# Optimization experiments

Measured on AMD Instinct MI355X. Metric: run time of the kernel, lower is better.

## Reference

```python
import jax, jax.numpy as jnp
import numpy as np

B = 64        # batch_size (conf.loader.batch_size)
N = 128       # points per graph
RATIO = 32    # aggregator nodes per graph
H = 8         # n_heads
HD = 64       # head dim = in_channels
E = H * HD    # embed dim = in_channels * n_heads = 512


def setup_inputs() -> dict:
    key = jax.random.key(0)
    ks = jax.random.split(key, 5)
    x = jax.random.normal(ks[0], (B, N, E), dtype=jnp.float32)
    # per-node graph ids, matching the row-major reshape of x: node i -> graph i // N
    batch = jnp.repeat(jnp.arange(B, dtype=jnp.int32), N)  # (B*N,)
    # learned aggregator seeds: torch.normal(0, 1, size=(ratio, E))
    aggrs = jax.random.normal(ks[1], (RATIO, E), dtype=jnp.float32)
    # MultiheadAttention params (torch layout: in_proj_weight (3E, E), out_proj (E, E))
    in_proj_w = jax.random.normal(ks[2], (3 * E, E), dtype=jnp.float32) / np.sqrt(E)
    in_proj_b = jnp.zeros((3 * E,), dtype=jnp.float32)
    out_proj_w = jax.random.normal(ks[3], (E, E), dtype=jnp.float32) / np.sqrt(E)
    out_proj_b = jnpp if False else jnp.zeros((E,), dtype=jnp.float32)
    return {"x": x, "batch": batch, "aggrs": aggrs,
            "in_proj_w": in_proj_w, "in_proj_b": in_proj_b,
            "out_proj_w": out_proj_w, "out_proj_b": out_proj_b}


def reference(x, batch, aggrs, in_proj_w, in_proj_b, out_proj_w, out_proj_b):
    Bsz, n, F = x.shape                       # (64, 128, 512)
    L = Bsz * RATIO                           # 2048 aggregator queries
    x_large = x.reshape(-1, F)                # (S, E), S = B*N = 8192
    q_in = jnp.tile(aggrs, (Bsz, 1))          # (L, E): aggrs.repeat(batch_size, 1)

    Wq, Wk, Wv = jnp.split(in_proj_w, 3, axis=0)
    bq, bk, bv = jnp.split(in_proj_b, 3)
    q = (q_in @ Wq.T + bq).reshape(L, H, HD).transpose(1, 0, 2)      # (H, L, HD)
    k = (x_large @ Wk.T + bk).reshape(-1, H, HD).transpose(1, 0, 2)  # (H, S, HD)
    v = (x_large @ Wv.T + bv).reshape(-1, H, HD).transpose(1, 0, 2)  # (H, S, HD)

    scores = jnp.einsum('hld,hsd->hls', q, k) / np.float32(np.sqrt(HD))  # (H, L, S)
    # mask = ~eye(B).repeat_interleave(ratio, 1); mask[batch].T -> (L, S) bool, True = blocked.
    # Equivalent: query l (belonging to graph l // ratio) may attend node s iff batch[s] == l // ratio.
    aggr_graph = jnp.arange(L, dtype=batch.dtype) // RATIO           # (L,)
    allowed = aggr_graph[:, None] == batch[None, :]                  # (L, S)
    scores = jnp.where(allowed[None, :, :], scores, -jnp.inf)
    attn = jax.nn.softmax(scores, axis=-1)                           # (H, L, S)

    out = jnp.einsum('hls,hsd->hld', attn, v)                        # (H, L, HD)
    out = out.transpose(1, 0, 2).reshape(L, F) @ out_proj_w.T + out_proj_b
    return out.reshape(Bsz, RATIO, F)                                # (B, ratio, E)
```

## Files before the change

kernel.cpp:

```cpp
#include <hip/hip_runtime.h>

typedef __attribute__((ext_vector_type(8))) short short8;
typedef __attribute__((ext_vector_type(4))) float f32x4;

__device__ inline float bf2f(unsigned short u) {
    return __uint_as_float(((unsigned int)u) << 16);
}
__device__ inline unsigned short f2bf(float f) {
    unsigned int x = __float_as_uint(f);
    return (unsigned short)((x + 0x7fffu + ((x >> 16) & 1u)) >> 16);
}

template<bool F32>
__device__ inline short8 load8(const void* p, long i) {
    short8 r;
    if (F32) {
        const float* fp = (const float*)p + i;
        f32x4 a = *(const f32x4*)fp;
        f32x4 b = *(const f32x4*)(fp + 4);
#pragma unroll
        for (int j = 0; j < 4; ++j) { r[j] = (short)f2bf(a[j]); r[4 + j] = (short)f2bf(b[j]); }
    } else {
        r = *(const short8*)((const unsigned short*)p + i);
    }
    return r;
}

__global__ __launch_bounds__(256) void prep_kernel(
    const float* __restrict__ w_in, const float* __restrict__ Wo,
    const float* __restrict__ aggrs, const float* __restrict__ b_in,
    const float* __restrict__ x,
    unsigned short* __restrict__ wkv,
    unsigned short* __restrict__ wob,
    unsigned short* __restrict__ Qs,
    unsigned short* __restrict__ xb)
{
    if (blockIdx.x < 8) {
        const int tid = threadIdx.x;
        const int w = tid >> 6, lane = tid & 63, l15 = lane & 15, l4 = lane >> 4;
        const int col0 = blockIdx.x * 64 + w * 16;
        const float bq = b_in[col0 + l15];
        for (int rt = 0; rt < 2; ++rt) {
            f32x4 acc = {0.f, 0.f, 0.f, 0.f};
#pragma unroll
            for (int kk = 0; kk < 16; ++kk) {
                short8 a = load8<true>(aggrs, (long)(rt * 16 + l15) * 512 + kk * 32 + l4 * 8);
                short8 b = load8<true>(w_in, (long)(col0 + l15) * 512 + kk * 32 + l4 * 8);
                acc = __builtin_amdgcn_mfma_f32_16x16x32_bf16(a, b, acc, 0, 0, 0);
            }
#pragma unroll
            for (int r = 0; r < 4; ++r)
                Qs[(long)(rt * 16 + l4 * 4 + r) * 512 + col0 + l15] = f2bf(acc[r] + bq);
        }
        return;
    }
    long u = (long)(blockIdx.x - 8) * 256 + threadIdx.x;
    const float* src;
    unsigned short* dst;
    long base;
    if (u < 65536)        { src = w_in + (long)512 * 512; dst = wkv; base = u; }
    else if (u < 98304)   { src = Wo;  dst = wob; base = u - 65536; }
    else if (u < 622592)  { src = x;   dst = xb;  base = u - 98304; }
    else return;
    long i = base * 8;
    f32x4 a = *(const f32x4*)(src + i);
    f32x4 b = *(const f32x4*)(src + i + 4);
    short8 v;
#pragma unroll
    for (int j = 0; j < 4; ++j) { v[j] = (short)f2bf(a[j]); v[4 + j] = (short)f2bf(b[j]); }
    *(short8*)(dst + i) = v;
}

__global__ __launch_bounds__(256, 2) void kvattn_kernel(
    const unsigned short* __restrict__ xb,
    const unsigned short* __restrict__ wkv,
    const float* __restrict__ b_in,
    const unsigned short* __restrict__ Qs,
    unsigned short* __restrict__ Oh)
{
    const int g = blockIdx.x;
    const int h = blockIdx.y;
    const int tid = threadIdx.x;
    const int w = tid >> 6, lane = tid & 63, l15 = lane & 15, l4 = lane >> 4;

    __shared__ __align__(16) unsigned short Wstage[16][512];
    __shared__ __align__(16) unsigned short K_lds[128][72];
    __shared__ __align__(16) unsigned short Vt_lds[64][136];
    __shared__ __align__(16) float S_lds[32][132];
    __shared__ __align__(16) unsigned short P_lds[32][136];

    short8 a0[16], a1[16];
    {
        const long xrow0 = (long)(g * 128 + w * 32 + l15) * 512 + l4 * 8;
#pragma unroll
        for (int kk = 0; kk < 16; ++kk) a0[kk] = *(const short8*)(xb + xrow0 + kk * 32);
        const long xrow1 = xrow0 + 16 * 512;
#pragma unroll
        for (int kk = 0; kk < 16; ++kk) a1[kk] = *(const short8*)(xb + xrow1 + kk * 32);
    }

    for (int cb = 0; cb < 8; ++cb) {
        if (cb) __syncthreads();
        const int wrow = (cb < 4) ? (h * 64 + cb * 16) : (512 + h * 64 + (cb - 4) * 16);
#pragma unroll
        for (int j = 0; j < 4; ++j) {
            int c = tid + j * 256;
            int row = c >> 6;
            int col8 = c & 63;
            *(short8*)(&Wstage[row][(col8 ^ (row & 7)) * 8]) =
                *(const short8*)(wkv + (long)(wrow + row) * 512 + col8 * 8);
        }
        __syncthreads();
        const float bias = b_in[512 + wrow + l15];
#pragma unroll
        for (int rt = 0; rt < 2; ++rt) {
            f32x4 acc = {0.f, 0.f, 0.f, 0.f};
#pragma unroll
            for (int kk = 0; kk < 16; ++kk) {
                short8 b = *(const short8*)(&Wstage[l15][((kk * 4 + l4) ^ (l15 & 7)) * 8]);
                acc = __builtin_amdgcn_mfma_f32_16x16x32_bf16(rt ? a1[kk] : a0[kk], b, acc, 0, 0, 0);
            }
            const int node0 = w * 32 + rt * 16 + l4 * 4;
            if (cb < 4) {
                const int col = cb * 16 + l15;
#pragma unroll
                for (int r = 0; r < 4; ++r) K_lds[node0 + r][col] = f2bf(acc[r] + bias);
            } else {
                const int d = (cb - 4) * 16 + l15;
#pragma unroll
                for (int r = 0; r < 4; ++r) Vt_lds[d][node0 + r] = f2bf(acc[r] + bias);
            }
        }
    }
    __syncthreads();

    for (int lt = 0; lt < 2; ++lt) {
        const int l0 = lt * 16;
        short8 qa[2];
        qa[0] = *(const short8*)(Qs + (long)(l0 + l15) * 512 + h * 64 + l4 * 8);
        qa[1] = *(const short8*)(Qs + (long)(l0 + l15) * 512 + h * 64 + 32 + l4 * 8);
        for (int ct = 0; ct < 2; ++ct) {
            const int n0 = w * 32 + ct * 16;
            f32x4 acc = {0.f, 0.f, 0.f, 0.f};
#pragma unroll
            for (int kk = 0; kk < 2; ++kk) {
                short8 b = *(const short8*)(&K_lds[n0 + l15][kk * 32 + l4 * 8]);
                acc = __builtin_amdgcn_mfma_f32_16x16x32_bf16(qa[kk], b, acc, 0, 0, 0);
            }
#pragma unroll
            for (int r = 0; r < 4; ++r)
                S_lds[l0 + l4 * 4 + r][n0 + l15] = acc[r] * 0.125f;
        }
    }
    __syncthreads();

    {
        const int row = tid >> 3;
        const int j = tid & 7;
        float vals[16];
        float m = -1e30f;
#pragma unroll
        for (int c = 0; c < 16; ++c) {
            vals[c] = S_lds[row][j + c * 8];
            m = fmaxf(m, vals[c]);
        }
#pragma unroll
        for (int s = 1; s < 8; s <<= 1) m = fmaxf(m, __shfl_xor(m, s));
        float sum = 0.f;
#pragma unroll
        for (int c = 0; c < 16; ++c) {
            vals[c] = __expf(vals[c] - m);
            sum += vals[c];
        }
#pragma unroll
        for (int s = 1; s < 8; s <<= 1) sum += __shfl_xor(sum, s);
        const float inv = 1.0f / sum;
#pragma unroll
        for (int c = 0; c < 16; ++c)
            P_lds[row][j + c * 8] = f2bf(vals[c] * inv);
    }
    __syncthreads();

    for (int lt = 0; lt < 2; ++lt) {
        const int l0 = lt * 16;
        const int d0 = w * 16;
        f32x4 acc = {0.f, 0.f, 0.f, 0.f};
#pragma unroll
        for (int kk = 0; kk < 4; ++kk) {
            short8 a = *(const short8*)(&P_lds[l0 + l15][kk * 32 + l4 * 8]);
            short8 b = *(const short8*)(&Vt_lds[d0 + l15][kk * 32 + l4 * 8]);
            acc = __builtin_amdgcn_mfma_f32_16x16x32_bf16(a, b, acc, 0, 0, 0);
        }
#pragma unroll
        for (int r = 0; r < 4; ++r) {
            const int l = l0 + l4 * 4 + r;
            Oh[(long)h * 131072 + (long)(g * 32 + l) * 64 + d0 + l15] = f2bf(acc[r]);
        }
    }
}

__global__ __launch_bounds__(256, 2) void outproj2_kernel(
    const unsigned short* __restrict__ Oh, const unsigned short* __restrict__ wob,
    const float* __restrict__ bo, float* __restrict__ out)
{
    const int by = blockIdx.x;
    const int tid = threadIdx.x;
    const int w = tid >> 6, lane = tid & 63, l15 = lane & 15, l4 = lane >> 4;

    __shared__ __align__(16) unsigned short O_lds[16][520];

#pragma unroll
    for (int i = 0; i < 4; ++i) {
        int c2 = tid + i * 256;
        int row = c2 >> 6;
        int c = c2 & 63;
        int hh = c >> 3;
        int d = (c & 7) * 8;
        *(short8*)(&O_lds[row][c * 8]) =
            *(const short8*)(Oh + (long)hh * 131072 + (long)(by * 16 + row) * 64 + d);
    }
    __syncthreads();

    short8 a[16];
#pragma unroll
    for (int kk = 0; kk < 16; ++kk)
        a[kk] = *(const short8*)(&O_lds[l15][kk * 32 + l4 * 8]);

    const int cbase = w * 128;
    for (int ct = 0; ct < 8; ++ct) {
        const int col0 = cbase + ct * 16;
        f32x4 acc = {0.f, 0.f, 0.f, 0.f};
#pragma unroll
        for (int kk = 0; kk < 16; ++kk) {
            short8 b = *(const short8*)(wob + (long)(col0 + l15) * 512 + kk * 32 + l4 * 8);
            acc = __builtin_amdgcn_mfma_f32_16x16x32_bf16(a[kk], b, acc, 0, 0, 0);
        }
        const float bias = bo[col0 + l15];
#pragma unroll
        for (int r = 0; r < 4; ++r)
            out[(long)(by * 16 + l4 * 4 + r) * 512 + col0 + l15] = acc[r] + bias;
    }
}

template<bool F32>
__device__ void attn_body(const void* x, const void* w_in, const float* b_in,
                          const void* aggrs, float* O) {
    const int h = blockIdx.x;
    const int g = blockIdx.y;
    const int tid = threadIdx.x;
    const int w = tid >> 6, lane = tid & 63, l15 = lane & 15, l4 = lane >> 4;

    __shared__ __align__(16) unsigned short Q_lds[32][72];
    __shared__ __align__(16) unsigned short K_lds[128][72];
    __shared__ __align__(16) unsigned short Vt_lds[64][136];
    __shared__ __align__(16) float S_lds[32][132];
    __shared__ __align__(16) unsigned short P_lds[32][136];

    const long xg = (long)g * 128 * 512;
    const long WqO = (long)(h * 64) * 512;
    const long WkO = (long)(512 + h * 64) * 512;
    const long WvO = (long)(1024 + h * 64) * 512;

    {
        const int d0 = w * 16;
        const float bq = b_in[h * 64 + d0 + l15];
        for (int rt = 0; rt < 2; ++rt) {
            f32x4 acc = {0.f, 0.f, 0.f, 0.f};
#pragma unroll
            for (int kk = 0; kk < 16; ++kk) {
                short8 a = load8<F32>(aggrs, (long)(rt * 16 + l15) * 512 + l4 * 8 + kk * 32);
                short8 b = load8<F32>(w_in, WqO + (long)(d0 + l15) * 512 + l4 * 8 + kk * 32);
                acc = __builtin_amdgcn_mfma_f32_16x16x32_bf16(a, b, acc, 0, 0, 0);
            }
#pragma unroll
            for (int r = 0; r < 4; ++r)
                Q_lds[rt * 16 + l4 * 4 + r][d0 + l15] = f2bf(acc[r] + bq);
        }
    }
    for (int rt = 0; rt < 2; ++rt) {
        const int n0 = w * 32 + rt * 16;
        short8 a[16];
#pragma unroll
        for (int kk = 0; kk < 16; ++kk)
            a[kk] = load8<F32>(x, xg + (long)(n0 + l15) * 512 + l4 * 8 + kk * 32);
        for (int ct = 0; ct < 4; ++ct) {
            const int d0 = ct * 16;
            f32x4 accK = {0.f, 0.f, 0.f, 0.f};
            f32x4 accV = {0.f, 0.f, 0.f, 0.f};
#pragma unroll
            for (int kk = 0; kk < 16; ++kk) {
                short8 bk = load8<F32>(w_in, WkO + (long)(d0 + l15) * 512 + l4 * 8 + kk * 32);
                short8 bv = load8<F32>(w_in, WvO + (long)(d0 + l15) * 512 + l4 * 8 + kk * 32);
                accK = __builtin_amdgcn_mfma_f32_16x16x32_bf16(a[kk], bk, accK, 0, 0, 0);
                accV = __builtin_amdgcn_mfma_f32_16x16x32_bf16(a[kk], bv, accV, 0, 0, 0);
            }
            const float biasK = b_in[512 + h * 64 + d0 + l15];
            const float biasV = b_in[1024 + h * 64 + d0 + l15];
#pragma unroll
            for (int r = 0; r < 4; ++r) {
                const int row = n0 + l4 * 4 + r;
                const int col = d0 + l15;
                K_lds[row][col] = f2bf(accK[r] + biasK);
                Vt_lds[col][row] = f2bf(accV[r] + biasV);
            }
        }
    }
    __syncthreads();
    for (int lt = 0; lt < 2; ++lt) {
        const int l0 = lt * 16;
        short8 qa[2];
        qa[0] = *(const short8*)(&Q_lds[l0 + l15][l4 * 8]);
        qa[1] = *(const short8*)(&Q_lds[l0 + l15][32 + l4 * 8]);
        for (int ct = 0; ct < 2; ++ct) {
            const int n0 = w * 32 + ct * 16;
            f32x4 acc = {0.f, 0.f, 0.f, 0.f};
#pragma unroll
            for (int kk = 0; kk < 2; ++kk) {
                short8 b = *(const short8*)(&K_lds[n0 + l15][kk * 32 + l4 * 8]);
                acc = __builtin_amdgcn_mfma_f32_16x16x32_bf16(qa[kk], b, acc, 0, 0, 0);
            }
#pragma unroll
            for (int r = 0; r < 4; ++r)
                S_lds[l0 + l4 * 4 + r][n0 + l15] = acc[r] * 0.125f;
        }
    }
    __syncthreads();
    {
        const int row = tid >> 3;
        const int j = tid & 7;
        float vals[16];
        float m = -1e30f;
#pragma unroll
        for (int c = 0; c < 16; ++c) {
            vals[c] = S_lds[row][j + c * 8];
            m = fmaxf(m, vals[c]);
        }
#pragma unroll
        for (int s = 1; s < 8; s <<= 1) m = fmaxf(m, __shfl_xor(m, s));
        float sum = 0.f;
#pragma unroll
        for (int c = 0; c < 16; ++c) {
            vals[c] = __expf(vals[c] - m);
            sum += vals[c];
        }
#pragma unroll
        for (int s = 1; s < 8; s <<= 1) sum += __shfl_xor(sum, s);
        const float inv = 1.0f / sum;
#pragma unroll
        for (int c = 0; c < 16; ++c)
            P_lds[row][j + c * 8] = f2bf(vals[c] * inv);
    }
    __syncthreads();
    for (int lt = 0; lt < 2; ++lt) {
        const int l0 = lt * 16;
        const int d0 = w * 16;
        f32x4 acc = {0.f, 0.f, 0.f, 0.f};
#pragma unroll
        for (int kk = 0; kk < 4; ++kk) {
            short8 a = *(const short8*)(&P_lds[l0 + l15][kk * 32 + l4 * 8]);
            short8 b = *(const short8*)(&Vt_lds[d0 + l15][kk * 32 + l4 * 8]);
            acc = __builtin_amdgcn_mfma_f32_16x16x32_bf16(a, b, acc, 0, 0, 0);
        }
#pragma unroll
        for (int r = 0; r < 4; ++r) {
            const int l = l0 + l4 * 4 + r;
            O[(long)(g * 32 + l) * 512 + h * 64 + d0 + l15] = acc[r];
        }
    }
}
__global__ __launch_bounds__(256) void attn_f32(const float* x, const float* w_in,
                                                const float* b_in, const float* aggrs,
                                                float* O) {
    attn_body<true>(x, w_in, b_in, aggrs, O);
}

template<bool F32>
__device__ void outproj_body(float* Out, const void* Wo, const float* bo) {
    const int by = blockIdx.x;
    const int tid = threadIdx.x;
    const int w = tid >> 6, lane = tid & 63, l15 = lane & 15, l4 = lane >> 4;

    __shared__ __align__(16) unsigned short O_lds[16][520];

#pragma unroll
    for (int i = 0; i < 4; ++i) {
        int c2 = tid + i * 256;
        int row = c2 >> 6;
        int col = (c2 & 63) * 8;
        const float* src = Out + (long)(by * 16 + row) * 512 + col;
        f32x4 a = *(const f32x4*)src;
        f32x4 b = *(const f32x4*)(src + 4);
        short8 v;
#pragma unroll
        for (int j = 0; j < 4; ++j) { v[j] = (short)f2bf(a[j]); v[4 + j] = (short)f2bf(b[j]); }
        *(short8*)(&O_lds[row][col]) = v;
    }
    __syncthreads();

    short8 a[16];
#pragma unroll
    for (int kk = 0; kk < 16; ++kk)
        a[kk] = *(const short8*)(&O_lds[l15][kk * 32 + l4 * 8]);

    const int cbase = w * 128;
    for (int ct = 0; ct < 8; ++ct) {
        const int col0 = cbase + ct * 16;
        f32x4 acc = {0.f, 0.f, 0.f, 0.f};
#pragma unroll
        for (int kk = 0; kk < 16; ++kk) {
            short8 b = load8<F32>(Wo, (long)(col0 + l15) * 512 + l4 * 8 + kk * 32);
            acc = __builtin_amdgcn_mfma_f32_16x16x32_bf16(a[kk], b, acc, 0, 0, 0);
        }
        const float bias = bo[col0 + l15];
#pragma unroll
        for (int r = 0; r < 4; ++r)
            Out[(long)(by * 16 + l4 * 4 + r) * 512 + col0 + l15] = acc[r] + bias;
    }
}
__global__ __launch_bounds__(256) void outproj_f32(float* Out, const float* Wo,
                                                   const float* bo) {
    outproj_body<true>(Out, Wo, bo);
}

extern "C" void kernel_launch(void* const* d_in, const int* in_sizes, int n_in,
                              void* d_out, int out_size, void* d_ws, size_t ws_size,
                              hipStream_t stream) {
    const int want[7] = {64 * 128 * 512, 64 * 128, 32 * 512, 1536 * 512, 1536, 512 * 512, 512};
    const void* p[7] = {0, 0, 0, 0, 0, 0, 0};
    for (int i = 0; i < n_in && i < 16; ++i)
        for (int j = 0; j < 7; ++j)
            if (in_sizes[i] == want[j] && p[j] == 0) { p[j] = d_in[i]; break; }

    const float* x     = (const float*)p[0];
    const float* aggrs = (const float*)p[2];
    const float* w_in  = (const float*)p[3];
    const float* b_in  = (const float*)p[4];
    const float* Wo    = (const float*)p[5];
    const float* bo    = (const float*)p[6];
    float* out = (float*)d_out;

    const size_t WKV = 0;
    const size_t WOB = 524288;
    const size_t QSo = 786432;
    const size_t XB  = 802816;
    const size_t OHo = 4997120;
    const size_t END = 6045696;

    unsigned short* ws = (unsigned short*)d_ws;
    if (ws_size >= END * 2) {
        prep_kernel<<<dim3(2440), dim3(256), 0, stream>>>(w_in, Wo, aggrs, b_in, x,
                                                          ws + WKV, ws + WOB, ws + QSo,
                                                          ws + XB);
        kvattn_kernel<<<dim3(64, 8), dim3(256), 0, stream>>>(ws + XB, ws + WKV, b_in,
                                                             ws + QSo, ws + OHo);
        outproj2_kernel<<<dim3(128), dim3(256), 0, stream>>>(ws + OHo, ws + WOB, bo, out);
    } else {
        attn_f32<<<dim3(8, 64), dim3(256), 0, stream>>>(x, w_in, b_in, aggrs, out);
        outproj_f32<<<dim3(128), dim3(256), 0, stream>>>(out, Wo, bo);
    }
}
```

Measured before the change: 67.51 us.

## Fuse bf16 conversion and Q projection into attention and out-proj kernels

Removes the separate prep kernel that converted x, the K/V weights and Wo to bf16 and computed the Q projection. The attention kernel now reads fp32 x and weights directly, converts them in registers, and computes its head's Q slice into LDS. Wstage and S_lds share one LDS arena region. This drops a launch and the round trip of the bf16 copies through memory, but every (graph, head) block now recomputes Q and re-converts the same x rows and weights, which means twice the global bytes per load.

```diff
diff --git a/kernel.cpp b/kernel.cpp
--- a/kernel.cpp
+++ b/kernel.cpp
@@ -26,56 +26,11 @@
     return r;
 }
 
-__global__ __launch_bounds__(256) void prep_kernel(
-    const float* __restrict__ w_in, const float* __restrict__ Wo,
-    const float* __restrict__ aggrs, const float* __restrict__ b_in,
+__global__ __launch_bounds__(256, 2) void kvattn_full_kernel(
     const float* __restrict__ x,
-    unsigned short* __restrict__ wkv,
-    unsigned short* __restrict__ wob,
-    unsigned short* __restrict__ Qs,
-    unsigned short* __restrict__ xb)
-{
-    if (blockIdx.x < 8) {
-        const int tid = threadIdx.x;
-        const int w = tid >> 6, lane = tid & 63, l15 = lane & 15, l4 = lane >> 4;
-        const int col0 = blockIdx.x * 64 + w * 16;
-        const float bq = b_in[col0 + l15];
-        for (int rt = 0; rt < 2; ++rt) {
-            f32x4 acc = {0.f, 0.f, 0.f, 0.f};
-#pragma unroll
-            for (int kk = 0; kk < 16; ++kk) {
-                short8 a = load8<true>(aggrs, (long)(rt * 16 + l15) * 512 + kk * 32 + l4 * 8);
-                short8 b = load8<true>(w_in, (long)(col0 + l15) * 512 + kk * 32 + l4 * 8);
-                acc = __builtin_amdgcn_mfma_f32_16x16x32_bf16(a, b, acc, 0, 0, 0);
-            }
-#pragma unroll
-            for (int r = 0; r < 4; ++r)
-                Qs[(long)(rt * 16 + l4 * 4 + r) * 512 + col0 + l15] = f2bf(acc[r] + bq);
-        }
-        return;
-    }
-    long u = (long)(blockIdx.x - 8) * 256 + threadIdx.x;
-    const float* src;
-    unsigned short* dst;
-    long base;
-    if (u < 65536)        { src = w_in + (long)512 * 512; dst = wkv; base = u; }
-    else if (u < 98304)   { src = Wo;  dst = wob; base = u - 65536; }
-    else if (u < 622592)  { src = x;   dst = xb;  base = u - 98304; }
-    else return;
-    long i = base * 8;
-    f32x4 a = *(const f32x4*)(src + i);
-    f32x4 b = *(const f32x4*)(src + i + 4);
-    short8 v;
-#pragma unroll
-    for (int j = 0; j < 4; ++j) { v[j] = (short)f2bf(a[j]); v[4 + j] = (short)f2bf(b[j]); }
-    *(short8*)(dst + i) = v;
-}
-
-__global__ __launch_bounds__(256, 2) void kvattn_kernel(
-    const unsigned short* __restrict__ xb,
-    const unsigned short* __restrict__ wkv,
+    const float* __restrict__ w_in,
     const float* __restrict__ b_in,
-    const unsigned short* __restrict__ Qs,
+    const float* __restrict__ aggrs,
     unsigned short* __restrict__ Oh)
 {
     const int g = blockIdx.x;
@@ -83,20 +38,39 @@
     const int tid = threadIdx.x;
     const int w = tid >> 6, lane = tid & 63, l15 = lane & 15, l4 = lane >> 4;
 
-    __shared__ __align__(16) unsigned short Wstage[16][512];
-    __shared__ __align__(16) unsigned short K_lds[128][72];
-    __shared__ __align__(16) unsigned short Vt_lds[64][136];
-    __shared__ __align__(16) float S_lds[32][132];
-    __shared__ __align__(16) unsigned short P_lds[32][136];
+    __shared__ __align__(16) unsigned char arena[66048];
+    unsigned short (*Q_lds)[72]    = (unsigned short(*)[72])(arena);
+    unsigned short (*K_lds)[72]    = (unsigned short(*)[72])(arena + 4608);
+    unsigned short (*Vt_lds)[136]  = (unsigned short(*)[136])(arena + 23040);
+    unsigned short (*P_lds)[136]   = (unsigned short(*)[136])(arena + 40448);
+    unsigned short (*Wstage)[512]  = (unsigned short(*)[512])(arena + 49152);
+    float          (*S_lds)[132]   = (float(*)[132])(arena + 49152);
+
+    {
+        const int d0 = w * 16;
+        const float bq = b_in[h * 64 + d0 + l15];
+        for (int rt = 0; rt < 2; ++rt) {
+            f32x4 acc = {0.f, 0.f, 0.f, 0.f};
+#pragma unroll
+            for (int kk = 0; kk < 16; ++kk) {
+                short8 a = load8<true>(aggrs, (long)(rt * 16 + l15) * 512 + kk * 32 + l4 * 8);
+                short8 b = load8<true>(w_in, (long)(h * 64 + d0 + l15) * 512 + kk * 32 + l4 * 8);
+                acc = __builtin_amdgcn_mfma_f32_16x16x32_bf16(a, b, acc, 0, 0, 0);
+            }
+#pragma unroll
+            for (int r = 0; r < 4; ++r)
+                Q_lds[rt * 16 + l4 * 4 + r][d0 + l15] = f2bf(acc[r] + bq);
+        }
+    }
 
     short8 a0[16], a1[16];
     {
         const long xrow0 = (long)(g * 128 + w * 32 + l15) * 512 + l4 * 8;
 #pragma unroll
-        for (int kk = 0; kk < 16; ++kk) a0[kk] = *(const short8*)(xb + xrow0 + kk * 32);
+        for (int kk = 0; kk < 16; ++kk) a0[kk] = load8<true>(x, xrow0 + kk * 32);
         const long xrow1 = xrow0 + 16 * 512;
 #pragma unroll
-        for (int kk = 0; kk < 16; ++kk) a1[kk] = *(const short8*)(xb + xrow1 + kk * 32);
+        for (int kk = 0; kk < 16; ++kk) a1[kk] = load8<true>(x, xrow1 + kk * 32);
     }
 
     for (int cb = 0; cb < 8; ++cb) {
@@ -108,7 +82,7 @@
             int row = c >> 6;
             int col8 = c & 63;
             *(short8*)(&Wstage[row][(col8 ^ (row & 7)) * 8]) =
-                *(const short8*)(wkv + (long)(wrow + row) * 512 + col8 * 8);
+                load8<true>(w_in, (long)(512 + wrow + row) * 512 + col8 * 8);
         }
         __syncthreads();
         const float bias = b_in[512 + wrow + l15];
@@ -137,8 +111,8 @@
     for (int lt = 0; lt < 2; ++lt) {
         const int l0 = lt * 16;
         short8 qa[2];
-        qa[0] = *(const short8*)(Qs + (long)(l0 + l15) * 512 + h * 64 + l4 * 8);
-        qa[1] = *(const short8*)(Qs + (long)(l0 + l15) * 512 + h * 64 + 32 + l4 * 8);
+        qa[0] = *(const short8*)(&Q_lds[l0 + l15][l4 * 8]);
+        qa[1] = *(const short8*)(&Q_lds[l0 + l15][32 + l4 * 8]);
         for (int ct = 0; ct < 2; ++ct) {
             const int n0 = w * 32 + ct * 16;
             f32x4 acc = {0.f, 0.f, 0.f, 0.f};
@@ -199,8 +173,8 @@
     }
 }
 
-__global__ __launch_bounds__(256, 2) void outproj2_kernel(
-    const unsigned short* __restrict__ Oh, const unsigned short* __restrict__ wob,
+__global__ __launch_bounds__(256, 2) void outproj2f_kernel(
+    const unsigned short* __restrict__ Oh, const float* __restrict__ Wo,
     const float* __restrict__ bo, float* __restrict__ out)
 {
     const int by = blockIdx.x;
@@ -232,7 +206,7 @@
         f32x4 acc = {0.f, 0.f, 0.f, 0.f};
 #pragma unroll
         for (int kk = 0; kk < 16; ++kk) {
-            short8 b = *(const short8*)(wob + (long)(col0 + l15) * 512 + kk * 32 + l4 * 8);
+            short8 b = load8<true>(Wo, (long)(col0 + l15) * 512 + kk * 32 + l4 * 8);
             acc = __builtin_amdgcn_mfma_f32_16x16x32_bf16(a[kk], b, acc, 0, 0, 0);
         }
         const float bias = bo[col0 + l15];
@@ -439,21 +413,10 @@
     const float* bo    = (const float*)p[6];
     float* out = (float*)d_out;
 
-    const size_t WKV = 0;
-    const size_t WOB = 524288;
-    const size_t QSo = 786432;
-    const size_t XB  = 802816;
-    const size_t OHo = 4997120;
-    const size_t END = 6045696;
-
-    unsigned short* ws = (unsigned short*)d_ws;
-    if (ws_size >= END * 2) {
-        prep_kernel<<<dim3(2440), dim3(256), 0, stream>>>(w_in, Wo, aggrs, b_in, x,
-                                                          ws + WKV, ws + WOB, ws + QSo,
-                                                          ws + XB);
-        kvattn_kernel<<<dim3(64, 8), dim3(256), 0, stream>>>(ws + XB, ws + WKV, b_in,
-                                                             ws + QSo, ws + OHo);
-        outproj2_kernel<<<dim3(128), dim3(256), 0, stream>>>(ws + OHo, ws + WOB, bo, out);
+    unsigned short* Oh = (unsigned short*)d_ws;
+    if (ws_size >= (size_t)8 * 2048 * 64 * 2) {
+        kvattn_full_kernel<<<dim3(64, 8), dim3(256), 0, stream>>>(x, w_in, b_in, aggrs, Oh);
+        outproj2f_kernel<<<dim3(128), dim3(256), 0, stream>>>(Oh, Wo, bo, out);
     } else {
         attn_f32<<<dim3(8, 64), dim3(256), 0, stream>>>(x, w_in, b_in, aggrs, out);
         outproj_f32<<<dim3(128), dim3(256), 0, stream>>>(out, Wo, bo);
```

Result: slower. 118.0 us (+74.8%).
